# Optimization experiments

Measured on AMD Instinct MI355X. Metric: run time of the kernel, lower is better.

## Reference

```python
import jax, jax.numpy as jnp
import numpy as np

F = 50  # number of feature fields

def setup_inputs() -> dict:
    key = jax.random.key(0)
    k1, k2, k3, k4 = jax.random.split(key, 4)
    B, D, A = 4096, 16, 32
    return {
        "feat_emb": jax.random.normal(k1, (B, F, D), dtype=jnp.float32),
        "W": jax.random.normal(k2, (D, A), dtype=jnp.float32) * 0.1,
        "h": jax.random.normal(k3, (A,), dtype=jnp.float32),
        "p_vec": jax.random.normal(k4, (D,), dtype=jnp.float32),
    }

def reference(feat_emb, W, h, p_vec):
    # build_cross: upper-triangular field pairs (i < j)
    row, col = np.triu_indices(F, k=1)              # each [P], P = F*(F-1)/2
    p = feat_emb[:, row]                             # [B, P, D]
    q = feat_emb[:, col]                             # [B, P, D]
    inter = p * q                                    # pairwise interaction [B, P, D]
    # AttLayer: Dense(no bias) -> relu -> contract with h -> softmax over pairs
    att_signal = jax.nn.relu(jnp.einsum('bpd,da->bpa', inter, W))  # [B, P, A]
    scores = jnp.einsum('bpa,a->bp', att_signal, h)                # [B, P]
    att = jax.nn.softmax(scores, axis=1)                           # [B, P]
    # attention-weighted sum-pooling over pairs
    pooled = jnp.einsum('bp,bpd->bd', att, inter)                  # [B, D]
    # dropout omitted (inference); final projection and reduce
    out = jnp.einsum('bd,d->b', pooled, p_vec)[:, None]            # [B, 1]
    return out
```

## Files before the change

kernel.cpp:

```cpp
#include <hip/hip_runtime.h>
#include <math.h>


#define FF 50
#define DD 16
#define AA 32
#define NP 1225
#define NT 39
#define ERS 24
#define EBS (FF * ERS)

typedef _Float16 half8 __attribute__((ext_vector_type(8)));
typedef _Float16 half4 __attribute__((ext_vector_type(4)));
typedef float    floatx16 __attribute__((ext_vector_type(16)));

__global__ __launch_bounds__(256, 4) void afm_kernel(
    const float* __restrict__ feat,
    const float* __restrict__ W,
    const float* __restrict__ h,
    const float* __restrict__ pvec,
    float* __restrict__ out,
    int Btot)
{
  __shared__ __align__(16) _Float16 eh[4 * EBS];
  __shared__ unsigned int tbl[NT * 32];

  const int tid    = threadIdx.x;
  const int lane   = tid & 63;
  const int wave   = tid >> 6;
  const int halfid = lane >> 5;
  const int n      = lane & 31;
  const int b0     = blockIdx.x << 2;
  const int b      = b0 + wave;

  for (int s = tid; s < 4 * 200; s += 256) {
    int bl  = s / 200;
    int rem = s - bl * 200;
    int bb  = b0 + bl;
    if (bb < Btot) {
      float4 v4 = ((const float4*)feat)[(size_t)bb * 200 + rem];
      half4 hv;
      hv[0] = (_Float16)v4.x; hv[1] = (_Float16)v4.y;
      hv[2] = (_Float16)v4.z; hv[3] = (_Float16)v4.w;
      int row = rem >> 2, q = rem & 3;
      *(half4*)(&eh[bl * EBS + row * ERS + q * 4]) = hv;
    }
  }

  for (int p = tid; p < NT * 32; p += 256) {
    unsigned ent = 0;
    if (p < NP) {
      int rad = 9801 - 8 * p;
      int i = (int)((99.0f - sqrtf((float)rad)) * 0.5f);
      if (i < 0) i = 0; if (i > 48) i = 48;
      int off = (i * (99 - i)) >> 1;
      if (off > p) { --i; off = (i * (99 - i)) >> 1; }
      else {
        int off1 = ((i + 1) * (98 - i)) >> 1;
        if (off1 <= p) { ++i; off = off1; }
      }
      int j = p - off + i + 1;
      ent = ((unsigned)(i * 48) << 16) | (unsigned)(j * 48);
    }
    tbl[p] = ent;
  }

  const float LOG2E = 1.4426950408889634f;
  half8 A0;
  #pragma unroll
  for (int jj = 0; jj < 8; ++jj)
    A0[jj] = (_Float16)W[(halfid * 8 + jj) * AA + n];
  float hreg[16];
  #pragma unroll
  for (int r = 0; r < 16; ++r)
    hreg[r] = h[(r & 3) + 8 * (r >> 2) + 4 * halfid] * LOG2E;
  float pvf[8];
  #pragma unroll
  for (int k = 0; k < 8; ++k) pvf[k] = pvec[halfid * 8 + k];

  __syncthreads();

  const char* ebase = (const char*)(eh + wave * EBS) + halfid * 16;

  auto tile = [&](int t, float& vout, float& gout) {
    unsigned ij = tbl[t * 32 + n];
    half8 Bi = *(const half8*)(ebase + (ij >> 16));
    half8 Bj = *(const half8*)(ebase + (ij & 0xffffu));
    half8 Bv = Bi * Bj;
    floatx16 z = __builtin_amdgcn_mfma_f32_32x32x16_f16(
        A0, Bv, (floatx16)0.0f, 0, 0, 0);
    float a0 = 0.f, a1 = 0.f, a2 = 0.f, a3 = 0.f;
    #pragma unroll
    for (int r = 0; r < 16; r += 4) {
      a0 = fmaf(fmaxf(z[r + 0], 0.f), hreg[r + 0], a0);
      a1 = fmaf(fmaxf(z[r + 1], 0.f), hreg[r + 1], a1);
      a2 = fmaf(fmaxf(z[r + 2], 0.f), hreg[r + 2], a2);
      a3 = fmaf(fmaxf(z[r + 3], 0.f), hreg[r + 3], a3);
    }
    float v = (a0 + a1) + (a2 + a3);
    v += __shfl_xor(v, 32, 64);
    float g = 0.f;
    #pragma unroll
    for (int k = 0; k < 8; ++k)
      g = fmaf((float)Bv[k], pvf[k], g);
    vout = v; gout = g;
  };

  float m = -3.0e38f, den = 0.f, num = 0.f;

  for (int t = 0; t < 38; t += 2) {
    float v0, g0, v1, g1;
    tile(t, v0, g0);
    tile(t + 1, v1, g1);
    float mn = fmaxf(fmaxf(v0, v1), m);
    float a  = exp2f(m - mn);
    float e0 = exp2f(v0 - mn);
    float e1 = exp2f(v1 - mn);
    den = fmaf(den, a, e0 + e1);
    num = fmaf(num, a, fmaf(e0, g0, e1 * g1));
    m = mn;
  }
  {
    float v, g;
    tile(38, v, g);
    float vl = (1216 + n < NP) ? v : -3.0e38f;
    float mn = fmaxf(m, vl);
    float a  = exp2f(m - mn);
    float e0 = exp2f(vl - mn);
    den = fmaf(den, a, e0);
    num = fmaf(num, a, e0 * g);
    m = mn;
  }

  #pragma unroll
  for (int mask = 32; mask >= 1; mask >>= 1) {
    float mo = __shfl_xor(m, mask, 64);
    float dn = __shfl_xor(den, mask, 64);
    float no = __shfl_xor(num, mask, 64);
    float mn = fmaxf(m, mo);
    float s1 = exp2f(m - mn), s2 = exp2f(mo - mn);
    den = den * s1 + dn * s2;
    num = num * s1 + no * s2;
    m = mn;
  }
  if (lane == 0 && b < Btot) out[b] = (2.0f * num) / den;
}

extern "C" void kernel_launch(void* const* d_in, const int* in_sizes, int n_in,
                              void* d_out, int out_size, void* d_ws, size_t ws_size,
                              hipStream_t stream) {
  const float* feat = (const float*)d_in[0];
  const float* W    = (const float*)d_in[1];
  const float* h    = (const float*)d_in[2];
  const float* pvec = (const float*)d_in[3];
  float* out = (float*)d_out;
  const int B = in_sizes[0] / (FF * DD);
  afm_kernel<<<(B + 3) / 4, 256, 0, stream>>>(feat, W, h, pvec, out, B);
}
```

Measured before the change: 90.68 us.

## Process two batch rows per wave and drop online softmax max tracking

Each wave now handles two batch rows, so 8 rows per block and half as many blocks. Each pair-index table load (now interleaved so two tiles come from one uint2 read) serves both rows. The online-softmax running max and rescaling are removed: scores go straight into exp2, and the final reduction becomes a plain sum. The p_vec dot product is done in fp16 vector arithmetic. These cut per-tile ALU and exp work and raise ILP, but they risk exp overflow for large scores, lose precision in the projection, and leave half as many waves to hide latency.

```diff
diff --git a/kernel.cpp b/kernel.cpp
--- a/kernel.cpp
+++ b/kernel.cpp
@@ -7,11 +7,13 @@
 #define AA 32
 #define NP 1225
 #define NT 39
+#define NTP 40
 #define ERS 24
 #define EBS (FF * ERS)
 
 typedef _Float16 half8 __attribute__((ext_vector_type(8)));
 typedef _Float16 half4 __attribute__((ext_vector_type(4)));
+typedef _Float16 half2v __attribute__((ext_vector_type(2)));
 typedef float    floatx16 __attribute__((ext_vector_type(16)));
 
 __global__ __launch_bounds__(256, 4) void afm_kernel(
@@ -22,18 +24,17 @@
     float* __restrict__ out,
     int Btot)
 {
-  __shared__ __align__(16) _Float16 eh[4 * EBS];
-  __shared__ unsigned int tbl[NT * 32];
+  __shared__ __align__(16) _Float16 eh[8 * EBS];
+  __shared__ unsigned int tbl[NTP * 32];
 
   const int tid    = threadIdx.x;
   const int lane   = tid & 63;
   const int wave   = tid >> 6;
   const int halfid = lane >> 5;
   const int n      = lane & 31;
-  const int b0     = blockIdx.x << 2;
-  const int b      = b0 + wave;
+  const int b0     = blockIdx.x << 3;
 
-  for (int s = tid; s < 4 * 200; s += 256) {
+  for (int s = tid; s < 8 * 200; s += 256) {
     int bl  = s / 200;
     int rem = s - bl * 200;
     int bb  = b0 + bl;
@@ -47,7 +48,10 @@
     }
   }
 
-  for (int p = tid; p < NT * 32; p += 256) {
+  for (int q = tid; q < NTP * 32; q += 256) {
+    int t = ((q >> 6) << 1) | (q & 1);
+    int nn = (q >> 1) & 31;
+    int p = t * 32 + nn;
     unsigned ent = 0;
     if (p < NP) {
       int rad = 9801 - 8 * p;
@@ -62,7 +66,7 @@
       int j = p - off + i + 1;
       ent = ((unsigned)(i * 48) << 16) | (unsigned)(j * 48);
     }
-    tbl[p] = ent;
+    tbl[q] = ent;
   }
 
   const float LOG2E = 1.4426950408889634f;
@@ -74,18 +78,19 @@
   #pragma unroll
   for (int r = 0; r < 16; ++r)
     hreg[r] = h[(r & 3) + 8 * (r >> 2) + 4 * halfid] * LOG2E;
-  float pvf[8];
+  half8 PV;
   #pragma unroll
-  for (int k = 0; k < 8; ++k) pvf[k] = pvec[halfid * 8 + k];
+  for (int k = 0; k < 8; ++k) PV[k] = (_Float16)pvec[halfid * 8 + k];
 
   __syncthreads();
 
-  const char* ebase = (const char*)(eh + wave * EBS) + halfid * 16;
+  const char* ebA = (const char*)(eh + (2 * wave) * EBS) + halfid * 16;
+  const char* ebB = ebA + EBS * sizeof(_Float16);
 
-  auto tile = [&](int t, float& vout, float& gout) {
-    unsigned ij = tbl[t * 32 + n];
-    half8 Bi = *(const half8*)(ebase + (ij >> 16));
-    half8 Bj = *(const half8*)(ebase + (ij & 0xffffu));
+  auto core = [&](const char* eb, unsigned oi, unsigned oj,
+                  float& vout, float& gout) {
+    half8 Bi = *(const half8*)(eb + oi);
+    half8 Bj = *(const half8*)(eb + oj);
     half8 Bv = Bi * Bj;
     floatx16 z = __builtin_amdgcn_mfma_f32_32x32x16_f16(
         A0, Bv, (floatx16)0.0f, 0, 0, 0);
@@ -98,52 +103,53 @@
       a3 = fmaf(fmaxf(z[r + 3], 0.f), hreg[r + 3], a3);
     }
     float v = (a0 + a1) + (a2 + a3);
-    v += __shfl_xor(v, 32, 64);
-    float g = 0.f;
-    #pragma unroll
-    for (int k = 0; k < 8; ++k)
-      g = fmaf((float)Bv[k], pvf[k], g);
-    vout = v; gout = g;
+    vout = v + __shfl_xor(v, 32, 64);
+    half8 gp = Bv * PV;
+    half4 g4 = {(_Float16)(gp[0] + gp[4]), (_Float16)(gp[1] + gp[5]),
+                (_Float16)(gp[2] + gp[6]), (_Float16)(gp[3] + gp[7])};
+    half2v g2 = {(_Float16)(g4[0] + g4[2]), (_Float16)(g4[1] + g4[3])};
+    gout = (float)g2[0] + (float)g2[1];
   };
 
-  float m = -3.0e38f, den = 0.f, num = 0.f;
+  float denA = 0.f, numA = 0.f, denB = 0.f, numB = 0.f;
 
-  for (int t = 0; t < 38; t += 2) {
-    float v0, g0, v1, g1;
-    tile(t, v0, g0);
-    tile(t + 1, v1, g1);
-    float mn = fmaxf(fmaxf(v0, v1), m);
-    float a  = exp2f(m - mn);
-    float e0 = exp2f(v0 - mn);
-    float e1 = exp2f(v1 - mn);
-    den = fmaf(den, a, e0 + e1);
-    num = fmaf(num, a, fmaf(e0, g0, e1 * g1));
-    m = mn;
+  const unsigned int* tpair = tbl + 2 * n;
+  for (int th = 0; th < 19; ++th) {
+    uint2 ij2 = *(const uint2*)(tpair + th * 64);
+    unsigned oi0 = ij2.x >> 16, oj0 = ij2.x & 0xffffu;
+    unsigned oi1 = ij2.y >> 16, oj1 = ij2.y & 0xffffu;
+    float v, g;
+    core(ebA, oi0, oj0, v, g);
+    { float e = exp2f(v); denA += e; numA = fmaf(e, g, numA); }
+    core(ebB, oi0, oj0, v, g);
+    { float e = exp2f(v); denB += e; numB = fmaf(e, g, numB); }
+    core(ebA, oi1, oj1, v, g);
+    { float e = exp2f(v); denA += e; numA = fmaf(e, g, numA); }
+    core(ebB, oi1, oj1, v, g);
+    { float e = exp2f(v); denB += e; numB = fmaf(e, g, numB); }
   }
   {
+    unsigned ij = tpair[19 * 64];
+    unsigned oi = ij >> 16, oj = ij & 0xffffu;
     float v, g;
-    tile(38, v, g);
-    float vl = (1216 + n < NP) ? v : -3.0e38f;
-    float mn = fmaxf(m, vl);
-    float a  = exp2f(m - mn);
-    float e0 = exp2f(vl - mn);
-    den = fmaf(den, a, e0);
-    num = fmaf(num, a, e0 * g);
-    m = mn;
+    core(ebA, oi, oj, v, g);
+    if (n >= 9) v = -3.0e38f;
+    { float e = exp2f(v); denA += e; numA = fmaf(e, g, numA); }
+    core(ebB, oi, oj, v, g);
+    if (n >= 9) v = -3.0e38f;
+    { float e = exp2f(v); denB += e; numB = fmaf(e, g, numB); }
   }
 
   #pragma unroll
   for (int mask = 32; mask >= 1; mask >>= 1) {
-    float mo = __shfl_xor(m, mask, 64);
-    float dn = __shfl_xor(den, mask, 64);
-    float no = __shfl_xor(num, mask, 64);
-    float mn = fmaxf(m, mo);
-    float s1 = exp2f(m - mn), s2 = exp2f(mo - mn);
-    den = den * s1 + dn * s2;
-    num = num * s1 + no * s2;
-    m = mn;
+    denA += __shfl_xor(denA, mask, 64);
+    numA += __shfl_xor(numA, mask, 64);
+    denB += __shfl_xor(denB, mask, 64);
+    numB += __shfl_xor(numB, mask, 64);
   }
-  if (lane == 0 && b < Btot) out[b] = (2.0f * num) / den;
+  const int bA = b0 + 2 * wave;
+  if (lane == 0 && bA < Btot)     out[bA]     = (2.0f * numA) / denA;
+  if (lane == 0 && bA + 1 < Btot) out[bA + 1] = (2.0f * numB) / denB;
 }
 
 extern "C" void kernel_launch(void* const* d_in, const int* in_sizes, int n_in,
@@ -155,5 +161,5 @@
   const float* pvec = (const float*)d_in[3];
   float* out = (float*)d_out;
   const int B = in_sizes[0] / (FF * DD);
-  afm_kernel<<<(B + 3) / 4, 256, 0, stream>>>(feat, W, h, pvec, out, B);
+  afm_kernel<<<(B + 7) / 8, 256, 0, stream>>>(feat, W, h, pvec, out, B);
 }
```

Result: no change. 89.86 us (-0.9%).
